# Performance work log

Measured on AMD Instinct MI355X. Metric: run time of the kernel, lower is better.

Reference implementation:

```python
import jax, jax.numpy as jnp
import numpy as np

NUM_HEADS = 4

def _proj(x, w, b):
    # Conv1d kernel_size=1 == pointwise linear over channels: [B, Cin, N] -> [B, Cout, N]
    return jnp.einsum('oi,bin->bon', w, x) + b[None, :, None]

def setup_inputs() -> dict:
    key = jax.random.key(0)
    ks = jax.random.split(key, 11)
    B, D, N = 8, 256, 2048
    inp = {
        'query': jax.random.normal(ks[0], (B, D, N), jnp.float32),
        'key':   jax.random.normal(ks[1], (B, D, N), jnp.float32),
        'value': jax.random.normal(ks[2], (B, D, N), jnp.float32),
        'w_q': jax.random.normal(ks[3], (D, D), jnp.float32) * (1.0 / np.sqrt(D)),
        'b_q': jax.random.normal(ks[4], (D,), jnp.float32) * 0.02,
        'w_k': jax.random.normal(ks[5], (D, D), jnp.float32) * (1.0 / np.sqrt(D)),
        'b_k': jax.random.normal(ks[6], (D,), jnp.float32) * 0.02,
        'w_v': jax.random.normal(ks[7], (D, D), jnp.float32) * (1.0 / np.sqrt(D)),
        'b_v': jax.random.normal(ks[8], (D,), jnp.float32) * 0.02,
        'w_m': jax.random.normal(ks[9], (D, D), jnp.float32) * (1.0 / np.sqrt(D)),
        'b_m': jax.random.normal(ks[10], (D,), jnp.float32) * 0.02,
    }
    return inp

def reference(query, key, value, w_q, b_q, w_k, b_k, w_v, b_v, w_m, b_m):
    B, D, N = query.shape
    H = NUM_HEADS
    d = D // H  # head dim (outer slot of channel split, matching torch .view)
    q = _proj(query, w_q, b_q).reshape(B, d, H, N)
    k = _proj(key,   w_k, b_k).reshape(B, d, H, N)
    v = _proj(value, w_v, b_v).reshape(B, d, H, N)
    scale = jnp.asarray(1.0 / np.sqrt(d), q.dtype)
    scores = jnp.einsum('bdhn,bdhm->bhnm', q, k) * scale  # [B,H,N,N]
    prob = jax.nn.softmax(scores, axis=-1)
    x = jnp.einsum('bhnm,bdhm->bdhn', prob, v)            # [B,d,H,N]
    out = _proj(x.reshape(B, D, N), w_m, b_m)             # [B,D,N]
    return out
```

## Files before the change

kernel.cpp:

```cpp
#include <hip/hip_runtime.h>
#include <cstdint>
#include <cstddef>

typedef unsigned short u16;
typedef unsigned int   u32;
typedef __attribute__((ext_vector_type(4))) float f32x4;
typedef __attribute__((ext_vector_type(16))) float f32x16;
typedef __attribute__((ext_vector_type(8))) short bf16x8;
typedef __attribute__((ext_vector_type(4))) unsigned short u16x4;
typedef __attribute__((ext_vector_type(2))) u32 u32x2;
typedef __attribute__((ext_vector_type(4))) u32 u32x4;

#define DEVI static __device__ __forceinline__
#define MFMA16(a,b,c) __builtin_amdgcn_mfma_f32_16x16x32_bf16((a),(b),(c),0,0,0)
#define MFMA32(a,b,c) __builtin_amdgcn_mfma_f32_32x32x16_bf16((a),(b),(c),0,0,0)
#define BAR()   __builtin_amdgcn_s_barrier()
#define CFENCE() asm volatile("" ::: "memory")

DEVI u16 f2b(float f) {
  u32 u = __builtin_bit_cast(u32, f);
  u32 r = u + 0x7fffu + ((u >> 16) & 1u);
  return (u16)(r >> 16);
}

DEVI u32 pkbf(float a, float b) {
  u32 r;
  asm("v_cvt_pk_bf16_f32 %0, %1, %2" : "=v"(r) : "v"(a), "v"(b));
  return r;
}

DEVI void load_lds16(const void* g, void* l) {
  __builtin_amdgcn_global_load_lds(
      (const __attribute__((address_space(1))) u32*)g,
      (__attribute__((address_space(3))) u32*)l, 16, 0, 0);
}

DEVI int perm_o(int o) { return 4 * (o & 63) + (o >> 6); }

__global__ __launch_bounds__(256) void k_prep_w(
    const float* __restrict__ wq, const float* __restrict__ wk,
    const float* __restrict__ wv, const float* __restrict__ wm,
    const float* __restrict__ bq, const float* __restrict__ bk, const float* __restrict__ bv,
    u16* __restrict__ WQ, u16* __restrict__ WK, u16* __restrict__ WV, u16* __restrict__ WM,
    float* __restrict__ BQ, float* __restrict__ BK, float* __restrict__ BV)
{
  int row = blockIdx.x, t = threadIdx.x, m = blockIdx.y;
  if (m == 0)      WQ[row * 256 + t] = f2b(wq[perm_o(row) * 256 + t]);
  else if (m == 1) WK[row * 256 + t] = f2b(wk[perm_o(row) * 256 + t]);
  else if (m == 2) WV[row * 256 + t] = f2b(wv[perm_o(row) * 256 + t]);
  else if (m == 3) WM[row * 256 + t] = f2b(wm[row * 256 + perm_o(t)]);
  else if (row == 0) {
    BQ[t] = bq[perm_o(t)];
    BK[t] = bk[perm_o(t)];
    BV[t] = bv[perm_o(t)];
  }
}

__global__ __launch_bounds__(256) void k_transpose(
    const float* __restrict__ q, const float* __restrict__ k, const float* __restrict__ v,
    u16* __restrict__ xq, u16* __restrict__ xk, u16* __restrict__ xv)
{
  __shared__ u16 tile[64][68];
  const int N = 2048, D = 256;
  int n0 = blockIdx.x * 64, c0 = blockIdx.y * 64;
  int b = blockIdx.z & 7, which = blockIdx.z >> 3;
  const float* src = (which == 0 ? q : which == 1 ? k : v) + (size_t)b * D * N;
  u16* dst = (which == 0 ? xq : which == 1 ? xk : xv) + (size_t)b * N * D;
  int t = threadIdx.x;
  int cl = t >> 4, ng = t & 15;
#pragma unroll
  for (int cc = 0; cc < 4; ++cc) {
    int c = cl + 16 * cc;
    f32x4 val = *(const f32x4*)&src[(size_t)(c0 + c) * N + n0 + ng * 4];
#pragma unroll
    for (int j = 0; j < 4; ++j) tile[c][ng * 4 + j] = f2b(val[j]);
  }
  __syncthreads();
  int n = t & 63, cq = t >> 6;
  union { u16 s[16]; u32x4 v4[2]; } pk;
#pragma unroll
  for (int j = 0; j < 16; ++j) pk.s[j] = tile[cq * 16 + j][n];
  u32x4* o = (u32x4*)&dst[(size_t)(n0 + n) * D + c0 + cq * 16];
  o[0] = pk.v4[0];
  o[1] = pk.v4[1];
}

template<int EPI>
__global__ __launch_bounds__(256, 4) void k_gemm(
    const u16* __restrict__ A, long sA,
    const u16* __restrict__ Bm, long sB,
    const float* __restrict__ bias,
    void* __restrict__ out, long sOut)
{
  __shared__ u16 lA[2][64 * 64];
  __shared__ u16 lB[2][64 * 64];
  int t = threadIdx.x, b = blockIdx.z;
  const u16* Ab = A + (size_t)b * sA + (size_t)blockIdx.x * 64 * 256;
  const u16* Bb = Bm + (size_t)b * sB + (size_t)blockIdx.y * 64 * 256;
  int l = t & 63, w = t >> 6, g = l >> 4, col = l & 15;
  int wr = w >> 1, wc = w & 1;
  f32x4 acc[2][2] = {};
  u32 sOf[2], sDs[2];
#pragma unroll
  for (int j = 0; j < 2; ++j) {
    int ci = t + 256 * j;
    int r = ci >> 3, c = ci & 7;
    sOf[j] = (u32)(r * 512 + ((c ^ (r & 7)) << 4));
    sDs[j] = (u32)(ci * 16);
  }
  auto stage = [&](int buf, int k0) {
#pragma unroll
    for (int j = 0; j < 2; ++j) {
      load_lds16((const char*)Ab + k0 * 2 + sOf[j], (char*)lA[buf] + sDs[j]);
      load_lds16((const char*)Bb + k0 * 2 + sOf[j], (char*)lB[buf] + sDs[j]);
    }
  };
  stage(0, 0);
  for (int s = 0; s < 4; ++s) {
    int cur = s & 1;
    if (s < 3) {
      stage(cur ^ 1, (s + 1) * 64);
      asm volatile("s_waitcnt vmcnt(4)" ::: "memory");
    } else {
      asm volatile("s_waitcnt vmcnt(0)" ::: "memory");
    }
    BAR(); CFENCE();
#pragma unroll
    for (int kc = 0; kc < 2; ++kc) {
      bf16x8 af[2], bfr[2];
#pragma unroll
      for (int mt = 0; mt < 2; ++mt) {
        int row = wr * 32 + mt * 16 + col;
        af[mt] = *(const bf16x8*)((const char*)lA[cur] + row * 128 + (((kc * 4 + g) ^ (row & 7)) << 4));
      }
#pragma unroll
      for (int nt = 0; nt < 2; ++nt) {
        int row = wc * 32 + nt * 16 + col;
        bfr[nt] = *(const bf16x8*)((const char*)lB[cur] + row * 128 + (((kc * 4 + g) ^ (row & 7)) << 4));
      }
#pragma unroll
      for (int mt = 0; mt < 2; ++mt)
#pragma unroll
        for (int nt = 0; nt < 2; ++nt)
          acc[mt][nt] = MFMA16(af[mt], bfr[nt], acc[mt][nt]);
    }
    if (s < 3) { CFENCE(); BAR(); }
  }
  if (EPI == 0) {
    u16* o = (u16*)out + (size_t)b * sOut;
#pragma unroll
    for (int nt = 0; nt < 2; ++nt) {
      int op = blockIdx.y * 64 + wc * 32 + nt * 16 + col;
      int hh = op >> 6, ii = op & 63;
      float bv = bias[op];
#pragma unroll
      for (int mt = 0; mt < 2; ++mt) {
        int nbase = blockIdx.x * 64 + wr * 32 + mt * 16 + g * 4;
#pragma unroll
        for (int r = 0; r < 4; ++r)
          o[((size_t)(hh * 2048 + nbase + r)) * 64 + ii] = f2b(acc[mt][nt][r] + bv);
      }
    }
  } else if (EPI == 1) {
    u16* o = (u16*)out + (size_t)b * sOut;
#pragma unroll
    for (int mt = 0; mt < 2; ++mt)
#pragma unroll
      for (int r = 0; r < 4; ++r) {
        int row = blockIdx.x * 64 + wr * 32 + mt * 16 + g * 4 + r;
        float bv = bias[row];
#pragma unroll
        for (int nt = 0; nt < 2; ++nt) {
          int cn = blockIdx.y * 64 + wc * 32 + nt * 16 + col;
          o[(size_t)row * 2048 + cn] = f2b(acc[mt][nt][r] + bv);
        }
      }
  } else {
    float* o = (float*)out + (size_t)b * sOut;
#pragma unroll
    for (int mt = 0; mt < 2; ++mt)
#pragma unroll
      for (int r = 0; r < 4; ++r) {
        int row = blockIdx.x * 64 + wr * 32 + mt * 16 + g * 4 + r;
        float bv = bias[row];
#pragma unroll
        for (int nt = 0; nt < 2; ++nt) {
          int cn = blockIdx.y * 64 + wc * 32 + nt * 16 + col;
          o[(size_t)row * 2048 + cn] = acc[mt][nt][r] + bv;
        }
      }
  }
}

__global__ __launch_bounds__(256, 2) void k_attn(
    const u16* __restrict__ Qt, const u16* __restrict__ Kt,
    const u16* __restrict__ Vw, u16* __restrict__ Xws)
{
  __shared__ u16 stg[2][2][4096];
  const float SC2 = 0.18033688011112042f;
  int t = threadIdx.x, l = t & 63;
  int w = t >> 6;
  int hi = l >> 5, col = l & 31;
  int nb = blockIdx.x, hh = blockIdx.y, b = blockIdx.z;
  const u16* Qb = Qt + ((size_t)(b * 4 + hh) * 2048) * 64;
  const u16* Kb = Kt + ((size_t)(b * 4 + hh) * 2048) * 64;
  const u16* Vb = Vw + ((size_t)(b * 256 + hh * 64)) * 2048;
  int nq = nb * 128 + w * 32 + col;

  bf16x8 qf[4];
#pragma unroll
  for (int ks = 0; ks < 4; ++ks)
    qf[ks] = *(const bf16x8*)&Qb[(size_t)nq * 64 + ks * 16 + hi * 8];

  u32 kSrc[2], vSrc[2], sDst[2];
#pragma unroll
  for (int j = 0; j < 2; ++j) {
    int ci = t + 256 * j;
    int r = ci >> 3, c = ci & 7;
    u32 sw = (u32)((c ^ ((r >> 2) & 7)) << 4);
    kSrc[j] = (u32)(r * 128) + sw;
    vSrc[j] = (u32)(r * 4096) + sw;
    sDst[j] = (u32)(ci * 16);
  }
  u32 offC[4];
#pragma unroll
  for (int ks = 0; ks < 4; ++ks)
    offC[ks] = (u32)(((2 * ks + hi) ^ ((col >> 2) & 7)) << 4);

  f32x16 xac0 = {}, xac1 = {};
  float psum = 0.0f, m_run = 0.0f;

  auto stage = [&](int buf, int tile) {
    const char* kb = (const char*)Kb + (size_t)tile * 8192;
    const char* vb = (const char*)Vb + (size_t)tile * 128;
#pragma unroll
    for (int j = 0; j < 2; ++j)
      load_lds16(kb + kSrc[j], (char*)stg[buf][0] + sDst[j]);
#pragma unroll
    for (int j = 0; j < 2; ++j)
      load_lds16(vb + vSrc[j], (char*)stg[buf][1] + sDst[j]);
  };

  stage(0, 0);
  for (int it = 0; it < 32; ++it) {
    int cur = it & 1;
    if (it < 31) {
      stage(cur ^ 1, it + 1);
      if (__any(psum > 16777216.0f)) {
        const float ds = 5.9604644775390625e-8f;
        xac0 *= ds; xac1 *= ds;
        psum *= ds;
        m_run += 24.0f;
      }
      asm volatile("s_waitcnt vmcnt(4)" ::: "memory");
    } else {
      asm volatile("s_waitcnt vmcnt(0)" ::: "memory");
    }
    BAR(); CFENCE();
    const char* kK = (const char*)stg[cur][0] + col * 128;
    const char* kV = (const char*)stg[cur][1] + col * 128;

    f32x16 sac0 = {}, sac1 = {};
    __builtin_amdgcn_s_setprio(1);
#pragma unroll
    for (int ks = 0; ks < 4; ++ks) {
      bf16x8 kf0 = *(const bf16x8*)(kK + offC[ks]);
      bf16x8 kf1 = *(const bf16x8*)(kK + 4096 + offC[ks]);
      sac0 = MFMA32(kf0, qf[ks], sac0);
      sac1 = MFMA32(kf1, qf[ks], sac1);
    }
    __builtin_amdgcn_s_setprio(0);

    bf16x8 pf[4];
#pragma unroll
    for (int mt = 0; mt < 2; ++mt) {
      const f32x16& sc = mt ? sac1 : sac0;
      float p[16];
#pragma unroll
      for (int r = 0; r < 16; ++r) {
        p[r] = __builtin_amdgcn_exp2f(__builtin_fmaf(sc[r], SC2, -m_run));
        psum += p[r];
      }
      u32 A0 = pkbf(p[0],  p[1]),  B0 = pkbf(p[2],  p[3]);
      u32 A1 = pkbf(p[4],  p[5]),  B1 = pkbf(p[6],  p[7]);
      u32 A2 = pkbf(p[8],  p[9]),  B2 = pkbf(p[10], p[11]);
      u32 A3 = pkbf(p[12], p[13]), B3 = pkbf(p[14], p[15]);
      asm("v_permlane32_swap_b32 %0, %1" : "+v"(A0), "+v"(A1));
      asm("v_permlane32_swap_b32 %0, %1" : "+v"(B0), "+v"(B1));
      asm("v_permlane32_swap_b32 %0, %1" : "+v"(A2), "+v"(A3));
      asm("v_permlane32_swap_b32 %0, %1" : "+v"(B2), "+v"(B3));
      union { u32 u[4]; bf16x8 v; } f0, f1;
      f0.u[0] = A0; f0.u[1] = B0; f0.u[2] = A1; f0.u[3] = B1;
      f1.u[0] = A2; f1.u[1] = B2; f1.u[2] = A3; f1.u[3] = B3;
      pf[mt * 2 + 0] = f0.v;
      pf[mt * 2 + 1] = f1.v;
    }

    __builtin_amdgcn_s_setprio(1);
#pragma unroll
    for (int S = 0; S < 4; ++S) {
      bf16x8 vf0 = *(const bf16x8*)(kV + offC[S]);
      bf16x8 vf1 = *(const bf16x8*)(kV + 4096 + offC[S]);
      xac0 = MFMA32(vf0, pf[S], xac0);
      xac1 = MFMA32(vf1, pf[S], xac1);
    }
    __builtin_amdgcn_s_setprio(0);
    if (it < 31) { CFENCE(); BAR(); }
  }

  psum += __shfl_xor(psum, 32);
  float inv = 1.0f / psum;
  u16* Ob = Xws + (size_t)b * 2048 * 256 + (size_t)nq * 256 + hh * 64;
#pragma unroll
  for (int it2 = 0; it2 < 2; ++it2) {
    const f32x16& xa = it2 ? xac1 : xac0;
#pragma unroll
    for (int rq = 0; rq < 4; ++rq) {
      float v0 = xa[4 * rq + 0] * inv;
      float v1 = xa[4 * rq + 1] * inv;
      float v2 = xa[4 * rq + 2] * inv;
      float v3 = xa[4 * rq + 3] * inv;
      u32x2 w2; w2[0] = pkbf(v0, v1); w2[1] = pkbf(v2, v3);
      *(u32x2*)&Ob[it2 * 32 + 8 * rq + 4 * hi] = w2;
    }
  }
}

extern "C" void kernel_launch(void* const* d_in, const int* in_sizes, int n_in,
                              void* d_out, int out_size, void* d_ws, size_t ws_size,
                              hipStream_t stream)
{
  const float* q_in = (const float*)d_in[0];
  const float* k_in = (const float*)d_in[1];
  const float* v_in = (const float*)d_in[2];
  const float* w_q  = (const float*)d_in[3];
  const float* b_q  = (const float*)d_in[4];
  const float* w_k  = (const float*)d_in[5];
  const float* b_k  = (const float*)d_in[6];
  const float* w_v  = (const float*)d_in[7];
  const float* b_v  = (const float*)d_in[8];
  const float* w_m  = (const float*)d_in[9];
  const float* b_m  = (const float*)d_in[10];

  char* ws = (char*)d_ws;
  u16* XT_Q = (u16*)(ws + 0);
  u16* XT_K = (u16*)(ws + 8388608);
  u16* XT_V = (u16*)(ws + 16777216);
  u16* QT   = (u16*)(ws + 25165824);
  u16* KT   = (u16*)(ws + 33554432);
  u16* VW   = (u16*)(ws + 41943040);
  u16* WQ   = (u16*)(ws + 50331648);
  u16* WK   = (u16*)(ws + 50462720);
  u16* WV   = (u16*)(ws + 50593792);
  u16* WM   = (u16*)(ws + 50724864);
  float* BQ = (float*)(ws + 50855936);
  float* BK = (float*)(ws + 50856960);
  float* BV = (float*)(ws + 50857984);

  k_prep_w<<<dim3(256, 5), 256, 0, stream>>>(w_q, w_k, w_v, w_m, b_q, b_k, b_v,
                                             WQ, WK, WV, WM, BQ, BK, BV);
  k_transpose<<<dim3(32, 4, 24), 256, 0, stream>>>(q_in, k_in, v_in, XT_Q, XT_K, XT_V);
  k_gemm<0><<<dim3(32, 4, 8), 256, 0, stream>>>(XT_Q, 2048L * 256, WQ, 0, BQ, QT, 4L * 2048 * 64);
  k_gemm<0><<<dim3(32, 4, 8), 256, 0, stream>>>(XT_K, 2048L * 256, WK, 0, BK, KT, 4L * 2048 * 64);
  k_gemm<1><<<dim3(4, 32, 8), 256, 0, stream>>>(WV, 0, XT_V, 2048L * 256, BV, VW, 256L * 2048);
  k_attn<<<dim3(16, 4, 8), 256, 0, stream>>>(QT, KT, VW, XT_Q);
  k_gemm<2><<<dim3(4, 32, 8), 256, 0, stream>>>(WM, 0, XT_Q, 2048L * 256, b_m, d_out, 256L * 2048);
}
```

Before: 105.9 us.

## Quad-buffer attention K/V staging, remap blocks per XCD, sum softmax via MFMA

The attention kernel goes from a 2-deep to a 4-deep LDS ring with prefetch distance 2, which lets it drop the trailing barrier in each iteration. The grid is flattened and remapped so that all blocks for one batch-head land on the same XCD, aiming at better L2 reuse of K/V. The per-lane softmax denominator accumulation and the final shuffle are replaced by an extra MFMA against a ones vector, and the LDS swizzle pattern changes. In exchange it doubles LDS use, which may cut occupancy, and the ring safety relies on the distance-2 prefetch avoiding overwrites without the removed barrier.

```diff
diff --git a/kernel.cpp b/kernel.cpp
--- a/kernel.cpp
+++ b/kernel.cpp
@@ -196,12 +196,16 @@
     const u16* __restrict__ Qt, const u16* __restrict__ Kt,
     const u16* __restrict__ Vw, u16* __restrict__ Xws)
 {
-  __shared__ u16 stg[2][2][4096];
+  __shared__ u16 stg[4][2][4096];
   const float SC2 = 0.18033688011112042f;
   int t = threadIdx.x, l = t & 63;
   int w = t >> 6;
   int hi = l >> 5, col = l & 31;
-  int nb = blockIdx.x, hh = blockIdx.y, b = blockIdx.z;
+  int lin = blockIdx.x;
+  int xcd = lin & 7, j = lin >> 3;
+  int bh = xcd * 4 + (j >> 4);
+  int nb = j & 15;
+  int b = bh >> 2, hh = bh & 3;
   const u16* Qb = Qt + ((size_t)(b * 4 + hh) * 2048) * 64;
   const u16* Kb = Kt + ((size_t)(b * 4 + hh) * 2048) * 64;
   const u16* Vb = Vw + ((size_t)(b * 256 + hh * 64)) * 2048;
@@ -214,44 +218,49 @@
 
   u32 kSrc[2], vSrc[2], sDst[2];
 #pragma unroll
-  for (int j = 0; j < 2; ++j) {
-    int ci = t + 256 * j;
+  for (int jj = 0; jj < 2; ++jj) {
+    int ci = t + 256 * jj;
     int r = ci >> 3, c = ci & 7;
-    u32 sw = (u32)((c ^ ((r >> 2) & 7)) << 4);
-    kSrc[j] = (u32)(r * 128) + sw;
-    vSrc[j] = (u32)(r * 4096) + sw;
-    sDst[j] = (u32)(ci * 16);
+    u32 sw = (u32)((c ^ ((r >> 1) & 7)) << 4);
+    kSrc[jj] = (u32)(r * 128) + sw;
+    vSrc[jj] = (u32)(r * 4096) + sw;
+    sDst[jj] = (u32)(ci * 16);
   }
   u32 offC[4];
 #pragma unroll
   for (int ks = 0; ks < 4; ++ks)
-    offC[ks] = (u32)(((2 * ks + hi) ^ ((col >> 2) & 7)) << 4);
-
-  f32x16 xac0 = {}, xac1 = {};
-  float psum = 0.0f, m_run = 0.0f;
+    offC[ks] = (u32)(((2 * ks + hi) ^ ((col >> 1) & 7)) << 4);
+
+  bf16x8 ones;
+  { union { u32 u[4]; bf16x8 v; } o; o.u[0] = o.u[1] = o.u[2] = o.u[3] = 0x3F803F80u; ones = o.v; }
+
+  f32x16 xac0 = {}, xac1 = {}, xsum = {};
+  float m_run = 0.0f;
 
   auto stage = [&](int buf, int tile) {
     const char* kb = (const char*)Kb + (size_t)tile * 8192;
     const char* vb = (const char*)Vb + (size_t)tile * 128;
 #pragma unroll
-    for (int j = 0; j < 2; ++j)
-      load_lds16(kb + kSrc[j], (char*)stg[buf][0] + sDst[j]);
-#pragma unroll
-    for (int j = 0; j < 2; ++j)
-      load_lds16(vb + vSrc[j], (char*)stg[buf][1] + sDst[j]);
+    for (int jj = 0; jj < 2; ++jj)
+      load_lds16(kb + kSrc[jj], (char*)stg[buf][0] + sDst[jj]);
+#pragma unroll
+    for (int jj = 0; jj < 2; ++jj)
+      load_lds16(vb + vSrc[jj], (char*)stg[buf][1] + sDst[jj]);
   };
 
   stage(0, 0);
+  stage(1, 1);
   for (int it = 0; it < 32; ++it) {
-    int cur = it & 1;
-    if (it < 31) {
-      stage(cur ^ 1, it + 1);
-      if (__any(psum > 16777216.0f)) {
+    int cur = it & 3;
+    if (it < 30) {
+      stage((it + 2) & 3, it + 2);
+      if (__any(xsum[0] > 16777216.0f)) {
         const float ds = 5.9604644775390625e-8f;
-        xac0 *= ds; xac1 *= ds;
-        psum *= ds;
+        xac0 *= ds; xac1 *= ds; xsum *= ds;
         m_run += 24.0f;
       }
+      asm volatile("s_waitcnt vmcnt(8)" ::: "memory");
+    } else if (it == 30) {
       asm volatile("s_waitcnt vmcnt(4)" ::: "memory");
     } else {
       asm volatile("s_waitcnt vmcnt(0)" ::: "memory");
@@ -277,10 +286,8 @@
       const f32x16& sc = mt ? sac1 : sac0;
       float p[16];
 #pragma unroll
-      for (int r = 0; r < 16; ++r) {
+      for (int r = 0; r < 16; ++r)
         p[r] = __builtin_amdgcn_exp2f(__builtin_fmaf(sc[r], SC2, -m_run));
-        psum += p[r];
-      }
       u32 A0 = pkbf(p[0],  p[1]),  B0 = pkbf(p[2],  p[3]);
       u32 A1 = pkbf(p[4],  p[5]),  B1 = pkbf(p[6],  p[7]);
       u32 A2 = pkbf(p[8],  p[9]),  B2 = pkbf(p[10], p[11]);
@@ -303,13 +310,12 @@
       bf16x8 vf1 = *(const bf16x8*)(kV + 4096 + offC[S]);
       xac0 = MFMA32(vf0, pf[S], xac0);
       xac1 = MFMA32(vf1, pf[S], xac1);
+      xsum = MFMA32(ones, pf[S], xsum);
     }
     __builtin_amdgcn_s_setprio(0);
-    if (it < 31) { CFENCE(); BAR(); }
-  }
-
-  psum += __shfl_xor(psum, 32);
-  float inv = 1.0f / psum;
+  }
+
+  float inv = 1.0f / xsum[0];
   u16* Ob = Xws + (size_t)b * 2048 * 256 + (size_t)nq * 256 + hh * 64;
 #pragma unroll
   for (int it2 = 0; it2 < 2; ++it2) {
@@ -363,6 +369,6 @@
   k_gemm<0><<<dim3(32, 4, 8), 256, 0, stream>>>(XT_Q, 2048L * 256, WQ, 0, BQ, QT, 4L * 2048 * 64);
   k_gemm<0><<<dim3(32, 4, 8), 256, 0, stream>>>(XT_K, 2048L * 256, WK, 0, BK, KT, 4L * 2048 * 64);
   k_gemm<1><<<dim3(4, 32, 8), 256, 0, stream>>>(WV, 0, XT_V, 2048L * 256, BV, VW, 256L * 2048);
-  k_attn<<<dim3(16, 4, 8), 256, 0, stream>>>(QT, KT, VW, XT_Q);
+  k_attn<<<dim3(512), 256, 0, stream>>>(QT, KT, VW, XT_Q);
   k_gemm<2><<<dim3(4, 32, 8), 256, 0, stream>>>(WM, 0, XT_Q, 2048L * 256, b_m, d_out, 256L * 2048);
 }
```

Result: no change. 106.4 us (+0.4%).

## Restructure attention kernel to 16x16 MFMA with smaller query tiles and XCD-aware grid

Applied to the files above, without the earlier changes.

The attention kernel now handles 64 queries per block (16 per wave) instead of 128 and uses 16x16x32 MFMAs instead of 32x32x16. The probability tile is passed to the PV MFMA through a swizzled LDS buffer rather than permlane swaps. The grid is flattened and remapped so each XCD handles a contiguous set of batch/head pairs for better L2 reuse, and launch bounds ask for 4 blocks per CU. This doubles the block count and should improve occupancy and cache locality. In exchange, K/V tiles are loaded twice as often per query, and each step adds an LDS round trip plus an extra barrier.

```diff
diff --git a/kernel.cpp b/kernel.cpp
--- a/kernel.cpp
+++ b/kernel.cpp
@@ -13,7 +13,6 @@
 
 #define DEVI static __device__ __forceinline__
 #define MFMA16(a,b,c) __builtin_amdgcn_mfma_f32_16x16x32_bf16((a),(b),(c),0,0,0)
-#define MFMA32(a,b,c) __builtin_amdgcn_mfma_f32_32x32x16_bf16((a),(b),(c),0,0,0)
 #define BAR()   __builtin_amdgcn_s_barrier()
 #define CFENCE() asm volatile("" ::: "memory")
 
@@ -192,53 +191,60 @@
   }
 }
 
-__global__ __launch_bounds__(256, 2) void k_attn(
+__global__ __launch_bounds__(256, 4) void k_attn(
     const u16* __restrict__ Qt, const u16* __restrict__ Kt,
     const u16* __restrict__ Vw, u16* __restrict__ Xws)
 {
   __shared__ u16 stg[2][2][4096];
+  __shared__ u16 lP[4][1024];
   const float SC2 = 0.18033688011112042f;
-  int t = threadIdx.x, l = t & 63;
-  int w = t >> 6;
-  int hi = l >> 5, col = l & 31;
-  int nb = blockIdx.x, hh = blockIdx.y, b = blockIdx.z;
+  int t = threadIdx.x, l = t & 63, w = t >> 6;
+  int g = l >> 4, col = l & 15;
+  int lin = blockIdx.x;
+  int xcd = lin & 7, jj = lin >> 3;
+  int bh = xcd * 4 + (jj >> 5), nb = jj & 31;
+  int b = bh >> 2, hh = bh & 3;
   const u16* Qb = Qt + ((size_t)(b * 4 + hh) * 2048) * 64;
   const u16* Kb = Kt + ((size_t)(b * 4 + hh) * 2048) * 64;
   const u16* Vb = Vw + ((size_t)(b * 256 + hh * 64)) * 2048;
-  int nq = nb * 128 + w * 32 + col;
-
-  bf16x8 qf[4];
-#pragma unroll
-  for (int ks = 0; ks < 4; ++ks)
-    qf[ks] = *(const bf16x8*)&Qb[(size_t)nq * 64 + ks * 16 + hi * 8];
+  int nq = nb * 64 + w * 16 + col;
+
+  bf16x8 qf0 = *(const bf16x8*)&Qb[(size_t)nq * 64 + g * 8];
+  bf16x8 qf1 = *(const bf16x8*)&Qb[(size_t)nq * 64 + 32 + g * 8];
 
   u32 kSrc[2], vSrc[2], sDst[2];
 #pragma unroll
-  for (int j = 0; j < 2; ++j) {
-    int ci = t + 256 * j;
+  for (int j2 = 0; j2 < 2; ++j2) {
+    int ci = t + 256 * j2;
     int r = ci >> 3, c = ci & 7;
-    u32 sw = (u32)((c ^ ((r >> 2) & 7)) << 4);
-    kSrc[j] = (u32)(r * 128) + sw;
-    vSrc[j] = (u32)(r * 4096) + sw;
-    sDst[j] = (u32)(ci * 16);
-  }
-  u32 offC[4];
-#pragma unroll
-  for (int ks = 0; ks < 4; ++ks)
-    offC[ks] = (u32)(((2 * ks + hi) ^ ((col >> 2) & 7)) << 4);
-
-  f32x16 xac0 = {}, xac1 = {};
+    u32 sw = (u32)((c ^ ((r >> 1) & 7)) << 4);
+    kSrc[j2] = (u32)(r * 128) + sw;
+    vSrc[j2] = (u32)(r * 4096) + sw;
+    sDst[j2] = (u32)(ci * 16);
+  }
+  u32 keyC = (u32)(col >> 1);
+  u32 offK[2];
+#pragma unroll
+  for (int kc = 0; kc < 2; ++kc)
+    offK[kc] = (u32)((((u32)(kc * 4 + g)) ^ keyC) << 4);
+  u32 colb = (u32)(col * 128);
+  u32 keyP = (u32)(col & 7);
+  u32 pW = (u32)(w * 2048 + col * 128 + (g & 1) * 8);
+  u32 pR = (u32)(w * 2048 + col * 128);
+  u32 cwBase = (u32)(g >> 1);
+
+  f32x4 xac[4] = {};
   float psum = 0.0f, m_run = 0.0f;
 
   auto stage = [&](int buf, int tile) {
     const char* kb = (const char*)Kb + (size_t)tile * 8192;
     const char* vb = (const char*)Vb + (size_t)tile * 128;
 #pragma unroll
-    for (int j = 0; j < 2; ++j)
-      load_lds16(kb + kSrc[j], (char*)stg[buf][0] + sDst[j]);
-#pragma unroll
-    for (int j = 0; j < 2; ++j)
-      load_lds16(vb + vSrc[j], (char*)stg[buf][1] + sDst[j]);
+    for (int j2 = 0; j2 < 2; ++j2)
+      load_lds16(kb + kSrc[j2], (char*)stg[buf][0] + sDst[j2]);
+#pragma unroll
+    for (int j2 = 0; j2 < 2; ++j2)
+      load_lds16(vb + vSrc[j2], (char*)stg[buf][1] + sDst[j2]);
   };
 
   stage(0, 0);
@@ -248,7 +254,8 @@
       stage(cur ^ 1, it + 1);
       if (__any(psum > 16777216.0f)) {
         const float ds = 5.9604644775390625e-8f;
-        xac0 *= ds; xac1 *= ds;
+#pragma unroll
+        for (int q4 = 0; q4 < 4; ++q4) xac[q4] *= ds;
         psum *= ds;
         m_run += 24.0f;
       }
@@ -257,72 +264,60 @@
       asm volatile("s_waitcnt vmcnt(0)" ::: "memory");
     }
     BAR(); CFENCE();
-    const char* kK = (const char*)stg[cur][0] + col * 128;
-    const char* kV = (const char*)stg[cur][1] + col * 128;
-
-    f32x16 sac0 = {}, sac1 = {};
+    const char* kK = (const char*)stg[cur][0] + colb;
+    const char* kV = (const char*)stg[cur][1] + colb;
+
+    f32x4 sacc[4] = {};
     __builtin_amdgcn_s_setprio(1);
 #pragma unroll
-    for (int ks = 0; ks < 4; ++ks) {
-      bf16x8 kf0 = *(const bf16x8*)(kK + offC[ks]);
-      bf16x8 kf1 = *(const bf16x8*)(kK + 4096 + offC[ks]);
-      sac0 = MFMA32(kf0, qf[ks], sac0);
-      sac1 = MFMA32(kf1, qf[ks], sac1);
+    for (int kc = 0; kc < 2; ++kc) {
+      bf16x8 qf = kc ? qf1 : qf0;
+#pragma unroll
+      for (int mt = 0; mt < 4; ++mt) {
+        bf16x8 kf = *(const bf16x8*)(kK + (u32)(mt * 2048) + offK[kc]);
+        sacc[mt] = MFMA16(kf, qf, sacc[mt]);
+      }
     }
     __builtin_amdgcn_s_setprio(0);
 
-    bf16x8 pf[4];
-#pragma unroll
-    for (int mt = 0; mt < 2; ++mt) {
-      const f32x16& sc = mt ? sac1 : sac0;
-      float p[16];
-#pragma unroll
-      for (int r = 0; r < 16; ++r) {
-        p[r] = __builtin_amdgcn_exp2f(__builtin_fmaf(sc[r], SC2, -m_run));
-        psum += p[r];
-      }
-      u32 A0 = pkbf(p[0],  p[1]),  B0 = pkbf(p[2],  p[3]);
-      u32 A1 = pkbf(p[4],  p[5]),  B1 = pkbf(p[6],  p[7]);
-      u32 A2 = pkbf(p[8],  p[9]),  B2 = pkbf(p[10], p[11]);
-      u32 A3 = pkbf(p[12], p[13]), B3 = pkbf(p[14], p[15]);
-      asm("v_permlane32_swap_b32 %0, %1" : "+v"(A0), "+v"(A1));
-      asm("v_permlane32_swap_b32 %0, %1" : "+v"(B0), "+v"(B1));
-      asm("v_permlane32_swap_b32 %0, %1" : "+v"(A2), "+v"(A3));
-      asm("v_permlane32_swap_b32 %0, %1" : "+v"(B2), "+v"(B3));
-      union { u32 u[4]; bf16x8 v; } f0, f1;
-      f0.u[0] = A0; f0.u[1] = B0; f0.u[2] = A1; f0.u[3] = B1;
-      f1.u[0] = A2; f1.u[1] = B2; f1.u[2] = A3; f1.u[3] = B3;
-      pf[mt * 2 + 0] = f0.v;
-      pf[mt * 2 + 1] = f1.v;
-    }
+    float ps = 0.0f;
+#pragma unroll
+    for (int mt = 0; mt < 4; ++mt) {
+      float p0 = __builtin_amdgcn_exp2f(__builtin_fmaf(sacc[mt][0], SC2, -m_run));
+      float p1 = __builtin_amdgcn_exp2f(__builtin_fmaf(sacc[mt][1], SC2, -m_run));
+      float p2 = __builtin_amdgcn_exp2f(__builtin_fmaf(sacc[mt][2], SC2, -m_run));
+      float p3 = __builtin_amdgcn_exp2f(__builtin_fmaf(sacc[mt][3], SC2, -m_run));
+      ps += (p0 + p1) + (p2 + p3);
+      u32x2 w2; w2[0] = pkbf(p0, p1); w2[1] = pkbf(p2, p3);
+      u32 cw = (u32)(mt * 2) + cwBase;
+      *(u32x2*)((char*)lP + pW + ((cw ^ keyP) << 4)) = w2;
+    }
+    psum += ps;
 
     __builtin_amdgcn_s_setprio(1);
 #pragma unroll
-    for (int S = 0; S < 4; ++S) {
-      bf16x8 vf0 = *(const bf16x8*)(kV + offC[S]);
-      bf16x8 vf1 = *(const bf16x8*)(kV + 4096 + offC[S]);
-      xac0 = MFMA32(vf0, pf[S], xac0);
-      xac1 = MFMA32(vf1, pf[S], xac1);
+    for (int S = 0; S < 2; ++S) {
+      bf16x8 pf = *(const bf16x8*)((char*)lP + pR + ((((u32)(S * 4 + g)) ^ keyP) << 4));
+#pragma unroll
+      for (int it2 = 0; it2 < 4; ++it2) {
+        bf16x8 vf = *(const bf16x8*)(kV + (u32)(it2 * 2048) + offK[S]);
+        xac[it2] = MFMA16(vf, pf, xac[it2]);
+      }
     }
     __builtin_amdgcn_s_setprio(0);
-    if (it < 31) { CFENCE(); BAR(); }
-  }
-
+    CFENCE(); BAR();
+  }
+
+  psum += __shfl_xor(psum, 16);
   psum += __shfl_xor(psum, 32);
   float inv = 1.0f / psum;
   u16* Ob = Xws + (size_t)b * 2048 * 256 + (size_t)nq * 256 + hh * 64;
 #pragma unroll
-  for (int it2 = 0; it2 < 2; ++it2) {
-    const f32x16& xa = it2 ? xac1 : xac0;
-#pragma unroll
-    for (int rq = 0; rq < 4; ++rq) {
-      float v0 = xa[4 * rq + 0] * inv;
-      float v1 = xa[4 * rq + 1] * inv;
-      float v2 = xa[4 * rq + 2] * inv;
-      float v3 = xa[4 * rq + 3] * inv;
-      u32x2 w2; w2[0] = pkbf(v0, v1); w2[1] = pkbf(v2, v3);
-      *(u32x2*)&Ob[it2 * 32 + 8 * rq + 4 * hi] = w2;
-    }
+  for (int it2 = 0; it2 < 4; ++it2) {
+    u32x2 w2;
+    w2[0] = pkbf(xac[it2][0] * inv, xac[it2][1] * inv);
+    w2[1] = pkbf(xac[it2][2] * inv, xac[it2][3] * inv);
+    *(u32x2*)&Ob[it2 * 16 + g * 4] = w2;
   }
 }
 
@@ -363,6 +358,6 @@
   k_gemm<0><<<dim3(32, 4, 8), 256, 0, stream>>>(XT_Q, 2048L * 256, WQ, 0, BQ, QT, 4L * 2048 * 64);
   k_gemm<0><<<dim3(32, 4, 8), 256, 0, stream>>>(XT_K, 2048L * 256, WK, 0, BK, KT, 4L * 2048 * 64);
   k_gemm<1><<<dim3(4, 32, 8), 256, 0, stream>>>(WV, 0, XT_V, 2048L * 256, BV, VW, 256L * 2048);
-  k_attn<<<dim3(16, 4, 8), 256, 0, stream>>>(QT, KT, VW, XT_Q);
+  k_attn<<<dim3(1024), 256, 0, stream>>>(QT, KT, VW, XT_Q);
   k_gemm<2><<<dim3(4, 32, 8), 256, 0, stream>>>(WM, 0, XT_Q, 2048L * 256, b_m, d_out, 256L * 2048);
 }
```

Result: slower. 116.5 us (+10.0%).

## Split attention KV range across wave pairs and merge partial softmax in LDS

Applied to the files above, without the earlier changes.

The attention kernel now gives each block 64 queries, not 128, and splits the 2048 keys into two halves handled by separate wave pairs. Each pair streams 32-key tiles, and the two pairs' partial accumulators, sums and running offsets are merged through an LDS union at the end. The grid becomes 1024 blocks with an XCD-aware linear mapping and launch bounds of 4 blocks per CU, aiming for more parallelism and occupancy. In exchange, each iteration does half as many MFMAs between barriers, and the kernel adds a combine step with extra LDS traffic.

```diff
diff --git a/kernel.cpp b/kernel.cpp
--- a/kernel.cpp
+++ b/kernel.cpp
@@ -192,53 +192,68 @@
   }
 }
 
-__global__ __launch_bounds__(256, 2) void k_attn(
+__global__ __launch_bounds__(256, 4) void k_attn(
     const u16* __restrict__ Qt, const u16* __restrict__ Kt,
     const u16* __restrict__ Vw, u16* __restrict__ Xws)
 {
-  __shared__ u16 stg[2][2][4096];
+  __shared__ union {
+    u16 stg[2][2][2][2048];
+    float cmb[2][64][34];
+  } sh;
   const float SC2 = 0.18033688011112042f;
-  int t = threadIdx.x, l = t & 63;
-  int w = t >> 6;
+  int t = threadIdx.x, l = t & 63, w = t >> 6;
   int hi = l >> 5, col = l & 31;
-  int nb = blockIdx.x, hh = blockIdx.y, b = blockIdx.z;
+  int qh = w & 1, kvh = w >> 1;
+  int lin = blockIdx.x;
+  int xcd = lin & 7, jj = lin >> 3;
+  int bh = xcd * 4 + (jj >> 5), nb = jj & 31;
+  int b = bh >> 2, hh = bh & 3;
   const u16* Qb = Qt + ((size_t)(b * 4 + hh) * 2048) * 64;
   const u16* Kb = Kt + ((size_t)(b * 4 + hh) * 2048) * 64;
   const u16* Vb = Vw + ((size_t)(b * 256 + hh * 64)) * 2048;
-  int nq = nb * 128 + w * 32 + col;
+  int nq = nb * 64 + qh * 32 + col;
 
   bf16x8 qf[4];
 #pragma unroll
   for (int ks = 0; ks < 4; ++ks)
     qf[ks] = *(const bf16x8*)&Qb[(size_t)nq * 64 + ks * 16 + hi * 8];
 
+  int tp = t & 127;
   u32 kSrc[2], vSrc[2], sDst[2];
 #pragma unroll
-  for (int j = 0; j < 2; ++j) {
-    int ci = t + 256 * j;
-    int r = ci >> 3, c = ci & 7;
-    u32 sw = (u32)((c ^ ((r >> 2) & 7)) << 4);
-    kSrc[j] = (u32)(r * 128) + sw;
-    vSrc[j] = (u32)(r * 4096) + sw;
-    sDst[j] = (u32)(ci * 16);
-  }
-  u32 offC[4];
+  for (int j2 = 0; j2 < 2; ++j2) {
+    int ci = tp + 128 * j2;
+    int rk = ci >> 3, ck = ci & 7;
+    kSrc[j2] = (u32)(rk * 128 + ((ck ^ ((rk >> 1) & 7)) << 4));
+    int rv = ci >> 2, cv = ci & 3;
+    vSrc[j2] = (u32)(rv * 4096 + ((cv ^ ((rv >> 1) & 3)) << 4));
+    sDst[j2] = (u32)(ci * 16);
+  }
+  u32 offK[4];
 #pragma unroll
   for (int ks = 0; ks < 4; ++ks)
-    offC[ks] = (u32)(((2 * ks + hi) ^ ((col >> 2) & 7)) << 4);
+    offK[ks] = (u32)(((2 * ks + hi) ^ ((col >> 1) & 7)) << 4);
+  u32 offV[2];
+#pragma unroll
+  for (int S = 0; S < 2; ++S)
+    offV[S] = (u32)(((S * 2 + hi) ^ ((col >> 1) & 3)) << 4);
+
+  char* stgK[2] = { (char*)sh.stg[kvh][0][0], (char*)sh.stg[kvh][1][0] };
+  char* stgV[2] = { (char*)sh.stg[kvh][0][1], (char*)sh.stg[kvh][1][1] };
 
   f32x16 xac0 = {}, xac1 = {};
   float psum = 0.0f, m_run = 0.0f;
 
   auto stage = [&](int buf, int tile) {
-    const char* kb = (const char*)Kb + (size_t)tile * 8192;
-    const char* vb = (const char*)Vb + (size_t)tile * 128;
-#pragma unroll
-    for (int j = 0; j < 2; ++j)
-      load_lds16(kb + kSrc[j], (char*)stg[buf][0] + sDst[j]);
-#pragma unroll
-    for (int j = 0; j < 2; ++j)
-      load_lds16(vb + vSrc[j], (char*)stg[buf][1] + sDst[j]);
+    size_t off = (size_t)(kvh * 1024 + tile * 32);
+    const char* kb = (const char*)(Kb + off * 64);
+    const char* vb = (const char*)(Vb + off);
+#pragma unroll
+    for (int j2 = 0; j2 < 2; ++j2)
+      load_lds16(kb + kSrc[j2], stgK[buf] + sDst[j2]);
+#pragma unroll
+    for (int j2 = 0; j2 < 2; ++j2)
+      load_lds16(vb + vSrc[j2], stgV[buf] + sDst[j2]);
   };
 
   stage(0, 0);
@@ -248,8 +263,7 @@
       stage(cur ^ 1, it + 1);
       if (__any(psum > 16777216.0f)) {
         const float ds = 5.9604644775390625e-8f;
-        xac0 *= ds; xac1 *= ds;
-        psum *= ds;
+        xac0 *= ds; xac1 *= ds; psum *= ds;
         m_run += 24.0f;
       }
       asm volatile("s_waitcnt vmcnt(4)" ::: "memory");
@@ -257,71 +271,82 @@
       asm volatile("s_waitcnt vmcnt(0)" ::: "memory");
     }
     BAR(); CFENCE();
-    const char* kK = (const char*)stg[cur][0] + col * 128;
-    const char* kV = (const char*)stg[cur][1] + col * 128;
-
-    f32x16 sac0 = {}, sac1 = {};
+    const char* kK = stgK[cur] + col * 128;
+    const char* kV = stgV[cur] + col * 64;
+
+    f32x16 sac = {};
     __builtin_amdgcn_s_setprio(1);
 #pragma unroll
     for (int ks = 0; ks < 4; ++ks) {
-      bf16x8 kf0 = *(const bf16x8*)(kK + offC[ks]);
-      bf16x8 kf1 = *(const bf16x8*)(kK + 4096 + offC[ks]);
-      sac0 = MFMA32(kf0, qf[ks], sac0);
-      sac1 = MFMA32(kf1, qf[ks], sac1);
+      bf16x8 kf = *(const bf16x8*)(kK + offK[ks]);
+      sac = MFMA32(kf, qf[ks], sac);
     }
     __builtin_amdgcn_s_setprio(0);
 
-    bf16x8 pf[4];
-#pragma unroll
-    for (int mt = 0; mt < 2; ++mt) {
-      const f32x16& sc = mt ? sac1 : sac0;
-      float p[16];
-#pragma unroll
-      for (int r = 0; r < 16; ++r) {
-        p[r] = __builtin_amdgcn_exp2f(__builtin_fmaf(sc[r], SC2, -m_run));
-        psum += p[r];
-      }
-      u32 A0 = pkbf(p[0],  p[1]),  B0 = pkbf(p[2],  p[3]);
-      u32 A1 = pkbf(p[4],  p[5]),  B1 = pkbf(p[6],  p[7]);
-      u32 A2 = pkbf(p[8],  p[9]),  B2 = pkbf(p[10], p[11]);
-      u32 A3 = pkbf(p[12], p[13]), B3 = pkbf(p[14], p[15]);
-      asm("v_permlane32_swap_b32 %0, %1" : "+v"(A0), "+v"(A1));
-      asm("v_permlane32_swap_b32 %0, %1" : "+v"(B0), "+v"(B1));
-      asm("v_permlane32_swap_b32 %0, %1" : "+v"(A2), "+v"(A3));
-      asm("v_permlane32_swap_b32 %0, %1" : "+v"(B2), "+v"(B3));
-      union { u32 u[4]; bf16x8 v; } f0, f1;
-      f0.u[0] = A0; f0.u[1] = B0; f0.u[2] = A1; f0.u[3] = B1;
-      f1.u[0] = A2; f1.u[1] = B2; f1.u[2] = A3; f1.u[3] = B3;
-      pf[mt * 2 + 0] = f0.v;
-      pf[mt * 2 + 1] = f1.v;
-    }
+    float p[16];
+#pragma unroll
+    for (int r = 0; r < 16; ++r) {
+      p[r] = __builtin_amdgcn_exp2f(__builtin_fmaf(sac[r], SC2, -m_run));
+      psum += p[r];
+    }
+    u32 A0 = pkbf(p[0],  p[1]),  B0 = pkbf(p[2],  p[3]);
+    u32 A1 = pkbf(p[4],  p[5]),  B1 = pkbf(p[6],  p[7]);
+    u32 A2 = pkbf(p[8],  p[9]),  B2 = pkbf(p[10], p[11]);
+    u32 A3 = pkbf(p[12], p[13]), B3 = pkbf(p[14], p[15]);
+    asm("v_permlane32_swap_b32 %0, %1" : "+v"(A0), "+v"(A1));
+    asm("v_permlane32_swap_b32 %0, %1" : "+v"(B0), "+v"(B1));
+    asm("v_permlane32_swap_b32 %0, %1" : "+v"(A2), "+v"(A3));
+    asm("v_permlane32_swap_b32 %0, %1" : "+v"(B2), "+v"(B3));
+    union { u32 u[4]; bf16x8 v; } f0, f1;
+    f0.u[0] = A0; f0.u[1] = B0; f0.u[2] = A1; f0.u[3] = B1;
+    f1.u[0] = A2; f1.u[1] = B2; f1.u[2] = A3; f1.u[3] = B3;
+    bf16x8 pf0 = f0.v, pf1 = f1.v;
 
     __builtin_amdgcn_s_setprio(1);
-#pragma unroll
-    for (int S = 0; S < 4; ++S) {
-      bf16x8 vf0 = *(const bf16x8*)(kV + offC[S]);
-      bf16x8 vf1 = *(const bf16x8*)(kV + 4096 + offC[S]);
-      xac0 = MFMA32(vf0, pf[S], xac0);
-      xac1 = MFMA32(vf1, pf[S], xac1);
+    {
+      bf16x8 va = *(const bf16x8*)(kV + offV[0]);
+      bf16x8 vb2 = *(const bf16x8*)(kV + 2048 + offV[0]);
+      xac0 = MFMA32(va, pf0, xac0);
+      xac1 = MFMA32(vb2, pf0, xac1);
+      bf16x8 vc = *(const bf16x8*)(kV + offV[1]);
+      bf16x8 vd = *(const bf16x8*)(kV + 2048 + offV[1]);
+      xac0 = MFMA32(vc, pf1, xac0);
+      xac1 = MFMA32(vd, pf1, xac1);
     }
     __builtin_amdgcn_s_setprio(0);
-    if (it < 31) { CFENCE(); BAR(); }
-  }
-
-  psum += __shfl_xor(psum, 32);
-  float inv = 1.0f / psum;
-  u16* Ob = Xws + (size_t)b * 2048 * 256 + (size_t)nq * 256 + hh * 64;
-#pragma unroll
-  for (int it2 = 0; it2 < 2; ++it2) {
-    const f32x16& xa = it2 ? xac1 : xac0;
-#pragma unroll
-    for (int rq = 0; rq < 4; ++rq) {
-      float v0 = xa[4 * rq + 0] * inv;
-      float v1 = xa[4 * rq + 1] * inv;
-      float v2 = xa[4 * rq + 2] * inv;
-      float v3 = xa[4 * rq + 3] * inv;
-      u32x2 w2; w2[0] = pkbf(v0, v1); w2[1] = pkbf(v2, v3);
-      *(u32x2*)&Ob[it2 * 32 + 8 * rq + 4 * hi] = w2;
+    CFENCE(); BAR();
+  }
+
+  __syncthreads();
+  if (kvh == 1) {
+    float* d = &sh.cmb[qh][l][0];
+#pragma unroll
+    for (int r = 0; r < 16; ++r) { d[r] = xac0[r]; d[16 + r] = xac1[r]; }
+    d[32] = psum; d[33] = m_run;
+  }
+  __syncthreads();
+  if (kvh == 0) {
+    const float* s = &sh.cmb[qh][l][0];
+    float m1 = s[33], ps1 = s[32];
+    float M = fmaxf(m_run, m1);
+    float fA = __builtin_amdgcn_exp2f(m_run - M);
+    float fB = __builtin_amdgcn_exp2f(m1 - M);
+    float den = psum * fA + ps1 * fB;
+    den += __shfl_xor(den, 32);
+    float inv = 1.0f / den;
+    u16* Ob = Xws + (size_t)b * 2048 * 256 + (size_t)nq * 256 + hh * 64;
+#pragma unroll
+    for (int it2 = 0; it2 < 2; ++it2) {
+      const f32x16& xa = it2 ? xac1 : xac0;
+#pragma unroll
+      for (int rq = 0; rq < 4; ++rq) {
+        float v0 = (xa[4 * rq + 0] * fA + s[it2 * 16 + 4 * rq + 0] * fB) * inv;
+        float v1 = (xa[4 * rq + 1] * fA + s[it2 * 16 + 4 * rq + 1] * fB) * inv;
+        float v2 = (xa[4 * rq + 2] * fA + s[it2 * 16 + 4 * rq + 2] * fB) * inv;
+        float v3 = (xa[4 * rq + 3] * fA + s[it2 * 16 + 4 * rq + 3] * fB) * inv;
+        u32x2 w2; w2[0] = pkbf(v0, v1); w2[1] = pkbf(v2, v3);
+        *(u32x2*)&Ob[it2 * 32 + 8 * rq + 4 * hi] = w2;
+      }
     }
   }
 }
@@ -363,6 +388,6 @@
   k_gemm<0><<<dim3(32, 4, 8), 256, 0, stream>>>(XT_Q, 2048L * 256, WQ, 0, BQ, QT, 4L * 2048 * 64);
   k_gemm<0><<<dim3(32, 4, 8), 256, 0, stream>>>(XT_K, 2048L * 256, WK, 0, BK, KT, 4L * 2048 * 64);
   k_gemm<1><<<dim3(4, 32, 8), 256, 0, stream>>>(WV, 0, XT_V, 2048L * 256, BV, VW, 256L * 2048);
-  k_attn<<<dim3(16, 4, 8), 256, 0, stream>>>(QT, KT, VW, XT_Q);
+  k_attn<<<dim3(1024), 256, 0, stream>>>(QT, KT, VW, XT_Q);
   k_gemm<2><<<dim3(4, 32, 8), 256, 0, stream>>>(WM, 0, XT_Q, 2048L * 256, b_m, d_out, 256L * 2048);
 }
```

After: 120.6 us. 13.8% more time.
